# Kernel optimization log

Measured on AMD Instinct MI355X. Metric: run time of the kernel, lower is better.

## Reference

```python
import jax, jax.numpy as jnp
import numpy as np
from jax import lax

DIM = 384
HEADS = 8

def setup_inputs() -> dict:
    key = jax.random.key(0)
    ks = jax.random.split(key, 7)
    B, C, H, W = 4, DIM, 128, 128
    x = jax.random.normal(ks[0], (B, C, H, W), dtype=jnp.float32)
    y = jax.random.normal(ks[1], (B, C, H, W), dtype=jnp.float32)
    s1 = 1.0 / np.sqrt(C)
    Wq = jax.random.normal(ks[2], (C, C), dtype=jnp.float32) * s1          # 1x1 conv [out,in]
    Wkv = jax.random.normal(ks[3], (2 * C, C), dtype=jnp.float32) * s1     # 1x1 conv
    Wdw = jax.random.normal(ks[4], (3 * C, 1, 3, 3), dtype=jnp.float32) * (1.0 / 3.0)  # depthwise 3x3
    Wproj = jax.random.normal(ks[5], (C, C), dtype=jnp.float32) * s1       # 1x1 conv
    temperature = jnp.ones((HEADS, 1, 1), dtype=jnp.float32)
    return {"x": x, "y": y, "Wq": Wq, "Wkv": Wkv, "Wdw": Wdw,
            "Wproj": Wproj, "temperature": temperature}


def _conv1x1(x, W):
    # x: [b,c,h,w], W: [o,c] -> [b,o,h,w]
    return jnp.einsum('bchw,oc->bohw', x, W)


def _l2norm(t, eps=1e-12):
    n = jnp.sqrt(jnp.sum(t * t, axis=-1, keepdims=True))
    return t / jnp.maximum(n, eps)


def reference(x, y, Wq, Wkv, Wdw, Wproj, temperature):
    b, c, h, w = x.shape
    q = _conv1x1(x, Wq)                     # [b,c,h,w]
    kv = _conv1x1(y, Wkv)                   # [b,2c,h,w]
    qkv = jnp.concatenate([q, kv], axis=1)  # [b,3c,h,w]
    qkv = lax.conv_general_dilated(
        qkv, Wdw, window_strides=(1, 1), padding='SAME',
        dimension_numbers=('NCHW', 'OIHW', 'NCHW'),
        feature_group_count=3 * c)
    q, k, v = jnp.split(qkv, 3, axis=1)
    cp = c // HEADS
    hw = h * w
    # b (head c) h w -> b head c (h w)
    q = q.reshape(b, HEADS, cp, hw)
    k = k.reshape(b, HEADS, cp, hw)
    v = v.reshape(b, HEADS, cp, hw)
    q = _l2norm(q)
    k = _l2norm(k)
    attn = jnp.einsum('bhcn,bhdn->bhcd', q, k) * temperature  # [b,head,cp,cp]
    attn = jax.nn.softmax(attn, axis=-1)
    out = jnp.einsum('bhcd,bhdn->bhcn', attn, v)              # [b,head,cp,hw]
    out = out.reshape(b, c, h, w)
    return _conv1x1(out, Wproj)
```

## Files before the change

### kernel.cpp

```cpp
#include <hip/hip_runtime.h>
#include <hip/hip_bf16.h>

#define DIM 384
#define HEADS 8
#define CP 48
#define NB 4
#define HIMG 128
#define WIMG 128
#define HW 16384

using bf16 = __hip_bfloat16;

typedef __attribute__((ext_vector_type(8))) short bf16x8;
typedef __attribute__((ext_vector_type(4))) float f32x4;

__device__ __forceinline__ float lo_bf(unsigned u){ union{unsigned i; float f;} c; c.i = u<<16; return c.f; }
__device__ __forceinline__ float hi_bf(unsigned u){ union{unsigned i; float f;} c; c.i = u & 0xffff0000u; return c.f; }
__device__ __forceinline__ bf16 f2bf(float v){ return __float2bfloat16(v); }
__device__ __forceinline__ unsigned short bfbits(float v){ union{ bf16 h; unsigned short u; } c; c.h = f2bf(v); return c.u; }
__device__ __forceinline__ float s2f(short s){ union{unsigned u; float f;} c; c.u = ((unsigned)(unsigned short)s) << 16; return c.f; }
__device__ __forceinline__ void cvt4(const short* p, float* o){
  uint2 u = *(const uint2*)p;
  o[0]=lo_bf(u.x); o[1]=hi_bf(u.x); o[2]=lo_bf(u.y); o[3]=hi_bf(u.y);
}

__device__ __forceinline__ float4 load4f(const float* p){ return *(const float4*)p; }
__device__ __forceinline__ float4 load4f(const bf16* p){
  uint2 u = *(const uint2*)p;
  float4 r; r.x = lo_bf(u.x); r.y = hi_bf(u.x); r.z = lo_bf(u.y); r.w = hi_bf(u.y); return r;
}

__device__ __forceinline__ void st(float* p, float v){ *p = v; }
__device__ __forceinline__ void st(bf16* p, float v){ *p = f2bf(v); }

#define GLD_LDS16(g, l) __builtin_amdgcn_global_load_lds( \
    (const __attribute__((address_space(1))) void*)(g), \
    (__attribute__((address_space(3))) void*)(l), 16, 0, 0)

__global__ __launch_bounds__(256) void convert_w(
    const float* __restrict__ Wq, const float* __restrict__ Wkv,
    bf16* __restrict__ Wq_bf, bf16* __restrict__ Wkv_bf)
{
  int idx = (blockIdx.x*256 + threadIdx.x) * 2;
  const int NQ = DIM*DIM;
  const int NKV = 2*DIM*DIM;
  if (idx < NQ) {
    unsigned u = (unsigned)bfbits(Wq[idx]) | ((unsigned)bfbits(Wq[idx+1]) << 16);
    *(unsigned*)(Wq_bf + idx) = u;
  } else {
    int j = idx - NQ;
    if (j < NKV) {
      unsigned u = (unsigned)bfbits(Wkv[j]) | ((unsigned)bfbits(Wkv[j+1]) << 16);
      *(unsigned*)(Wkv_bf + j) = u;
    }
  }
}

template<typename TIn>
__global__ __launch_bounds__(256) void transpose_cast(
    const TIn* __restrict__ in0, const TIn* __restrict__ in1,
    bf16* __restrict__ out0, bf16* __restrict__ out1,
    long inBatchStride, long outBatchStride)
{
  const int zb = blockIdx.z;
  const TIn* in = (zb < NB) ? in0 : in1;
  bf16* outp = (zb < NB) ? out0 : out1;
  const int b = zb & 3;
  const int n0 = blockIdx.x * 64;
  const int c0 = blockIdx.y * 64;
  const TIn* inb = in + (long)b * inBatchStride;
  bf16* outb = outp + (long)b * outBatchStride;

  __shared__ float tile[64][66];
  const int t = threadIdx.x;
#pragma unroll
  for (int i = 0; i < 4; ++i) {
    int g = i*256 + t;
    int r = g >> 4, c4 = g & 15;
    float4 v = load4f(inb + (long)(c0 + r)*HW + n0 + c4*4);
    tile[r][c4*4+0] = v.x; tile[r][c4*4+1] = v.y;
    tile[r][c4*4+2] = v.z; tile[r][c4*4+3] = v.w;
  }
  __syncthreads();
#pragma unroll
  for (int i = 0; i < 8; ++i) {
    int g = i*256 + t;
    int n = g >> 5, cu = g & 31;
    unsigned u = (unsigned)bfbits(tile[cu*2][n]) | ((unsigned)bfbits(tile[cu*2+1][n]) << 16);
    *(unsigned*)(outb + (long)(n0 + n)*DIM + c0 + cu*2) = u;
  }
}

template<typename TOut>
__global__ __launch_bounds__(256) void gemm_mfma(
    const bf16* __restrict__ A, long aStride,
    const bf16* __restrict__ Bt, TOut* __restrict__ C, int M, int K)
{
  const int b  = blockIdx.z;
  const int m0 = blockIdx.y * 128;
  const int n0 = blockIdx.x * 128;
  const bf16* Ab  = A  + (long)b * aStride;
  const bf16* Btb = Bt + (long)b * (long)HW * K;
  TOut* Cb = C + (long)b * (long)M * HW;

  __shared__ short As[128*64];
  __shared__ short Bs[128*64];

  const int t = threadIdx.x;
  const int w = t >> 6, lane = t & 63;
  const int quad = lane >> 4, l16 = lane & 15;
  const int wm = (w >> 1) * 64, wn = (w & 1) * 64;

  const bf16* gA[4]; const bf16* gB[4];
#pragma unroll
  for (int i = 0; i < 4; ++i) {
    int f = w*256 + i*64 + lane;
    int r = f >> 3, p = f & 7;
    int c = p ^ (r & 7);
    gA[i] = Ab  + (long)(m0 + r)*K + c*8;
    gB[i] = Btb + (long)(n0 + r)*K + c*8;
  }

  f32x4 acc[4][4] = {};

  for (int k0 = 0; k0 < K; k0 += 64) {
#pragma unroll
    for (int i = 0; i < 4; ++i) {
      GLD_LDS16(gA[i], As + (w*256 + i*64)*8);
      GLD_LDS16(gB[i], Bs + (w*256 + i*64)*8);
      gA[i] += 64; gB[i] += 64;
    }
    __syncthreads();
#pragma unroll
    for (int kk = 0; kk < 2; ++kk) {
      bf16x8 af[4], bfr[4];
      const int sw = (kk*4 + quad) ^ (l16 & 7);
#pragma unroll
      for (int mt = 0; mt < 4; ++mt) {
        af[mt]  = *(const bf16x8*)(As + (wm + mt*16 + l16)*64 + sw*8);
        bfr[mt] = *(const bf16x8*)(Bs + (wn + mt*16 + l16)*64 + sw*8);
      }
#pragma unroll
      for (int mt = 0; mt < 4; ++mt)
#pragma unroll
        for (int nt = 0; nt < 4; ++nt)
          acc[mt][nt] = __builtin_amdgcn_mfma_f32_16x16x32_bf16(af[mt], bfr[nt], acc[mt][nt], 0, 0, 0);
    }
    __syncthreads();
  }

#pragma unroll
  for (int mt = 0; mt < 4; ++mt)
#pragma unroll
    for (int nt = 0; nt < 4; ++nt)
#pragma unroll
      for (int j = 0; j < 4; ++j) {
        int row = m0 + wm + mt*16 + quad*4 + j;
        int col = n0 + wn + nt*16 + l16;
        st(Cb + (long)row*HW + col, acc[mt][nt][j]);
      }
}

__global__ __launch_bounds__(256, 6) void dwconv_inplace(
    bf16* __restrict__ qb, bf16* __restrict__ kvb,
    const float* __restrict__ Wdw, float* __restrict__ ssq)
{
  const int ch = blockIdx.x;
  const int b  = blockIdx.y;
  bf16* plane = (ch < DIM) ? qb + ((long)b*DIM + ch)*HW
                           : kvb + ((long)b*2*DIM + (ch - DIM))*HW;
  float w9[9];
#pragma unroll
  for (int i = 0; i < 9; ++i) w9[i] = Wdw[ch*9 + i];

  __shared__ short t_[66*140];
  __shared__ float wsum[4];
  const int t = threadIdx.x;

  if (t < 66) *(uint2*)&t_[t*140 + 128] = make_uint2(0u, 0u);

#pragma unroll
  for (int i = 0; i < 9; ++i) {
    int chunk = i*256 + t;
    if (chunk < 66*32) {
      int r = chunk >> 5, c8 = chunk & 31;
      int gh = r - 1;
      uint2 v = make_uint2(0u, 0u);
      if (gh >= 0) v = *(const uint2*)(plane + gh*128 + c8*4);
      *(uint2*)&t_[r*140 + c8*4] = v;
    }
  }
  __syncthreads();

  const int r  = t >> 2;
  const int q  = t & 3;
  const int c0 = q * 32;
  float ss = 0.f;
  unsigned outu[16];

  auto compute = [&]() {
    const short* rT = t_ + (r    )*140 + c0;
    const short* rM = t_ + (r + 1)*140 + c0;
    const short* rB = t_ + (r + 2)*140 + c0;
    float at[4], am[4], ab[4];
    cvt4(rT, at); cvt4(rM, am); cvt4(rB, ab);
    float lt, lm, lb;
    if (q == 0) { lt = lm = lb = 0.f; }
    else { lt = s2f(rT[-1]); lm = s2f(rM[-1]); lb = s2f(rB[-1]); }
#pragma unroll
    for (int jb = 0; jb < 32; jb += 4) {
      float bt[4], bm[4], bb[4];
      cvt4(rT + jb + 4, bt);
      cvt4(rM + jb + 4, bm);
      cvt4(rB + jb + 4, bb);
      float o0 = w9[0]*lt    + w9[1]*at[0] + w9[2]*at[1]
               + w9[3]*lm    + w9[4]*am[0] + w9[5]*am[1]
               + w9[6]*lb    + w9[7]*ab[0] + w9[8]*ab[1];
      float o1 = w9[0]*at[0] + w9[1]*at[1] + w9[2]*at[2]
               + w9[3]*am[0] + w9[4]*am[1] + w9[5]*am[2]
               + w9[6]*ab[0] + w9[7]*ab[1] + w9[8]*ab[2];
      float o2 = w9[0]*at[1] + w9[1]*at[2] + w9[2]*at[3]
               + w9[3]*am[1] + w9[4]*am[2] + w9[5]*am[3]
               + w9[6]*ab[1] + w9[7]*ab[2] + w9[8]*ab[3];
      float o3 = w9[0]*at[2] + w9[1]*at[3] + w9[2]*bt[0]
               + w9[3]*am[2] + w9[4]*am[3] + w9[5]*bm[0]
               + w9[6]*ab[2] + w9[7]*ab[3] + w9[8]*bb[0];
      ss += o0*o0 + o1*o1 + o2*o2 + o3*o3;
      outu[(jb>>1)  ] = (unsigned)bfbits(o0) | ((unsigned)bfbits(o1) << 16);
      outu[(jb>>1)+1] = (unsigned)bfbits(o2) | ((unsigned)bfbits(o3) << 16);
      lt = at[3]; lm = am[3]; lb = ab[3];
#pragma unroll
      for (int u2 = 0; u2 < 4; ++u2) { at[u2]=bt[u2]; am[u2]=bm[u2]; ab[u2]=bb[u2]; }
    }
  };

  compute();
  uint2 halo = make_uint2(0u, 0u);
  if (t < 64) halo = *(const uint2*)&t_[(64 + (t >> 5))*140 + (t & 31)*4];
  __syncthreads();

#pragma unroll
  for (int i2 = 0; i2 < 8; ++i2)
    *(uint2*)&t_[r*140 + c0 + i2*4] = *(uint2*)&outu[i2*2];
  __syncthreads();
#pragma unroll
  for (int i2 = 0; i2 < 4; ++i2) {
    int chunk = i2*256 + t;
    int orow = chunk >> 4, ocol = (chunk & 15)*8;
    uint2 lo = *(const uint2*)&t_[orow*140 + ocol];
    uint2 hi = *(const uint2*)&t_[orow*140 + ocol + 4];
    *(uint4*)(plane + (long)orow*128 + ocol) = make_uint4(lo.x, lo.y, hi.x, hi.y);
  }
  __syncthreads();

  if (t < 64) *(uint2*)&t_[(t >> 5)*140 + (t & 31)*4] = halo;
#pragma unroll
  for (int i2 = 0; i2 < 8; ++i2) {
    int chunk = i2*256 + t;
    int rr = chunk >> 5, c8 = chunk & 31;
    int gh = 65 + rr;
    uint2 v = make_uint2(0u, 0u);
    if (gh < 128) v = *(const uint2*)(plane + gh*128 + c8*4);
    *(uint2*)&t_[(rr + 2)*140 + c8*4] = v;
  }
  __syncthreads();

  compute();
  __syncthreads();
#pragma unroll
  for (int i2 = 0; i2 < 8; ++i2)
    *(uint2*)&t_[r*140 + c0 + i2*4] = *(uint2*)&outu[i2*2];
  __syncthreads();
#pragma unroll
  for (int i2 = 0; i2 < 4; ++i2) {
    int chunk = i2*256 + t;
    int orow = chunk >> 4, ocol = (chunk & 15)*8;
    uint2 lo = *(const uint2*)&t_[orow*140 + ocol];
    uint2 hi = *(const uint2*)&t_[orow*140 + ocol + 4];
    *(uint4*)(plane + (long)(64 + orow)*128 + ocol) = make_uint4(lo.x, lo.y, hi.x, hi.y);
  }

  if (ch < 2*DIM) {
#pragma unroll
    for (int off = 32; off; off >>= 1) ss += __shfl_down(ss, off);
    if ((t & 63) == 0) wsum[t >> 6] = ss;
    __syncthreads();
    if (t == 0) ssq[b*2*DIM + ch] = wsum[0]+wsum[1]+wsum[2]+wsum[3];
  }
}

__global__ __launch_bounds__(512) void s_mfma(
    const bf16* __restrict__ qd, const bf16* __restrict__ kd,
    float* __restrict__ Sp)
{
  const int split = blockIdx.x;
  const int h = blockIdx.y, b = blockIdx.z;
  const int t = threadIdx.x, w = t >> 6, lane = t & 63;
  const int quad = lane >> 4, l16 = lane & 15;
  const bf16* qp = qd + ((long)b*DIM + h*CP)*HW;
  const bf16* kp = kd + ((long)b*DIM + h*CP)*HW;
  const int nbase = (split*8 + w) * 256;

  f32x4 acc[3][3] = {};
  for (int ks = 0; ks < 8; ++ks) {
    const int n = nbase + ks*32 + quad*8;
    bf16x8 aq[3], bk[3];
#pragma unroll
    for (int i = 0; i < 3; ++i) {
      aq[i] = *(const bf16x8*)(qp + (long)(i*16 + l16)*HW + n);
      bk[i] = *(const bf16x8*)(kp + (long)(i*16 + l16)*HW + n);
    }
#pragma unroll
    for (int i = 0; i < 3; ++i)
#pragma unroll
      for (int j = 0; j < 3; ++j)
        acc[i][j] = __builtin_amdgcn_mfma_f32_16x16x32_bf16(aq[i], bk[j], acc[i][j], 0, 0, 0);
  }

  __shared__ float Sred[8][CP*CP];
#pragma unroll
  for (int i = 0; i < 3; ++i)
#pragma unroll
    for (int j = 0; j < 3; ++j)
#pragma unroll
      for (int rr = 0; rr < 4; ++rr)
        Sred[w][(i*16 + quad*4 + rr)*CP + j*16 + l16] = acc[i][j][rr];
  __syncthreads();

  float* out = Sp + (long)split*(NB*HEADS*CP*CP) + ((long)(b*HEADS + h))*CP*CP;
  for (int g = t; g < CP*CP; g += 512) {
    float s = 0.f;
#pragma unroll
    for (int ww = 0; ww < 8; ++ww) s += Sred[ww][g];
    out[g] = s;
  }
}

__global__ __launch_bounds__(64) void softmax_attn(
    float* __restrict__ Sp, const float* __restrict__ ssq,
    const float* __restrict__ temp)
{
  const int bhc = blockIdx.x;
  const int c = bhc % CP;
  const int h = (bhc / CP) % HEADS;
  const int b = bhc / (CP * HEADS);
  const int lane = threadIdx.x;
  const long rowoff = ((long)(b*HEADS + h))*CP*CP + c*CP;
  const float rq = rsqrtf(ssq[b*2*DIM + h*CP + c]);
  const float tmp = temp[h];
  float logit = -1e30f;
  if (lane < CP) {
    float s = 0.f;
#pragma unroll
    for (int sl = 0; sl < 8; ++sl) s += Sp[(long)sl*(NB*HEADS*CP*CP) + rowoff + lane];
    float rk = rsqrtf(ssq[b*2*DIM + DIM + h*CP + lane]);
    logit = s * rq * rk * tmp;
  }
  float m = logit;
#pragma unroll
  for (int off = 32; off; off >>= 1) m = fmaxf(m, __shfl_down(m, off));
  m = __shfl(m, 0);
  float e = (lane < CP) ? __expf(logit - m) : 0.f;
  float s = e;
#pragma unroll
  for (int off = 32; off; off >>= 1) s += __shfl_down(s, off);
  s = __shfl(s, 0);
  if (lane < CP) Sp[rowoff + lane] = e / s;
}

__global__ __launch_bounds__(256) void w2fold(
    const float* __restrict__ attn, const float* __restrict__ Wproj,
    bf16* __restrict__ W2)
{
  const int ot = blockIdx.x;
  const int h  = blockIdx.y;
  const int b  = blockIdx.z;
  __shared__ float at[CP][CP];
  __shared__ float wp[128][CP];
  const int t = threadIdx.x;
  const float* Ap = attn + ((long)(b*HEADS + h))*CP*CP;
#pragma unroll
  for (int i = 0; i < 9; ++i) {
    int idx = t + 256*i;
    at[idx / CP][idx % CP] = Ap[idx];
  }
#pragma unroll
  for (int i = 0; i < 24; ++i) {
    int idx = t + 256*i;
    int o = idx / CP, c = idx % CP;
    wp[o][c] = Wproj[(long)(ot*128 + o)*DIM + h*CP + c];
  }
  __syncthreads();
#pragma unroll
  for (int i = 0; i < 24; ++i) {
    int idx = t + 256*i;
    int o = idx / CP, d = idx % CP;
    float a = 0.f;
#pragma unroll
    for (int c = 0; c < CP; ++c) a += wp[o][c] * at[c][d];
    W2[((long)b*DIM + ot*128 + o)*DIM + h*CP + d] = f2bf(a);
  }
}

extern "C" void kernel_launch(void* const* d_in, const int* in_sizes, int n_in,
                              void* d_out, int out_size, void* d_ws, size_t ws_size,
                              hipStream_t stream) {
  const float* x     = (const float*)d_in[0];
  const float* y     = (const float*)d_in[1];
  const float* Wq    = (const float*)d_in[2];
  const float* Wkv   = (const float*)d_in[3];
  const float* Wdw   = (const float*)d_in[4];
  const float* Wproj = (const float*)d_in[5];
  const float* temp  = (const float*)d_in[6];
  float* out = (float*)d_out;

  char* ws = (char*)d_ws;
  const long SZ_T  = 50331648L;
  bf16* xT    = (bf16*)(ws + 0L);
  bf16* yT    = (bf16*)(ws + SZ_T);
  bf16* q_bf  = (bf16*)(ws + 2*SZ_T);
  bf16* kv_bf = (bf16*)(ws + 3*SZ_T);
  char* tail  = ws + 5*SZ_T;
  bf16* Wq_bf  = (bf16*)(tail);
  bf16* Wkv_bf = (bf16*)(tail + 294912L);
  float* Sp    = (float*)(tail);
  bf16* W2_bf  = (bf16*)(tail + 294912L);
  float* ssq   = (float*)(tail + 2359296L);
  bf16* vdT    = xT;
  bf16* vd     = kv_bf + (long)DIM*HW;

  convert_w<<<864, 256, 0, stream>>>(Wq, Wkv, Wq_bf, Wkv_bf);
  transpose_cast<float><<<dim3(HW/64, DIM/64, 8), 256, 0, stream>>>(
      x, y, xT, yT, (long)DIM*HW, (long)HW*DIM);
  gemm_mfma<bf16><<<dim3(HW/128, DIM/128, NB), 256, 0, stream>>>(
      Wq_bf, 0, xT, q_bf, DIM, DIM);
  gemm_mfma<bf16><<<dim3(HW/128, 2*DIM/128, NB), 256, 0, stream>>>(
      Wkv_bf, 0, yT, kv_bf, 2*DIM, DIM);
  dwconv_inplace<<<dim3(3*DIM, NB), 256, 0, stream>>>(q_bf, kv_bf, Wdw, ssq);
  transpose_cast<bf16><<<dim3(HW/64, DIM/64, NB), 256, 0, stream>>>(
      vd, nullptr, vdT, nullptr, (long)2*DIM*HW, (long)HW*DIM);
  s_mfma<<<dim3(8, HEADS, NB), 512, 0, stream>>>(q_bf, kv_bf, Sp);
  softmax_attn<<<dim3(NB*HEADS*CP), 64, 0, stream>>>(Sp, ssq, temp);
  w2fold<<<dim3(3, HEADS, NB), 256, 0, stream>>>(Sp, Wproj, W2_bf);
  gemm_mfma<float><<<dim3(HW/128, DIM/128, NB), 256, 0, stream>>>(
      W2_bf, (long)DIM*DIM, vdT, out, DIM, DIM);
}
```

Baseline: 568.3 us.

## Process whole dwconv plane in one pass with 512 threads and direct stores

The depthwise conv kernel now loads the full 128x128 bf16 plane plus zero halo into shared memory at once, using 512 threads, instead of two 64-row halves with halo carry-over. Each thread computes its 32 outputs and writes them straight to global memory as 16-byte stores, with no staging back through shared memory. This removes several barriers and the second load/compute phase. In exchange, shared memory per block grows to about 36 KB, which can limit how many blocks fit per CU. Padding the row with a left zero column removes the q==0 branch.

```diff
diff --git a/kernel.cpp b/kernel.cpp
--- a/kernel.cpp
+++ b/kernel.cpp
@@ -161,7 +161,7 @@
       }
 }
 
-__global__ __launch_bounds__(256, 6) void dwconv_inplace(
+__global__ __launch_bounds__(512, 8) void dwconv_inplace(
     bf16* __restrict__ qb, bf16* __restrict__ kvb,
     const float* __restrict__ Wdw, float* __restrict__ ssq)
 {
@@ -173,111 +173,78 @@
 #pragma unroll
   for (int i = 0; i < 9; ++i) w9[i] = Wdw[ch*9 + i];
 
-  __shared__ short t_[66*140];
-  __shared__ float wsum[4];
+  __shared__ short t_[130*140];
+  __shared__ float wsum[8];
   const int t = threadIdx.x;
 
-  if (t < 66) *(uint2*)&t_[t*140 + 128] = make_uint2(0u, 0u);
-
-#pragma unroll
-  for (int i = 0; i < 9; ++i) {
-    int chunk = i*256 + t;
-    if (chunk < 66*32) {
-      int r = chunk >> 5, c8 = chunk & 31;
-      int gh = r - 1;
-      uint2 v = make_uint2(0u, 0u);
-      if (gh >= 0) v = *(const uint2*)(plane + gh*128 + c8*4);
-      *(uint2*)&t_[r*140 + c8*4] = v;
-    }
+  uint2 v[8];
+#pragma unroll
+  for (int i = 0; i < 8; ++i) {
+    int chunk = i*512 + t;
+    int r = chunk >> 5, c8 = chunk & 31;
+    v[i] = *(const uint2*)(plane + r*128 + c8*4);
+  }
+
+  if (t < 74) {
+    int row = (t < 37) ? 0 : 129;
+    int c4 = (t < 37) ? t : (t - 37);
+    *(uint2*)&t_[row*140 + c4*4] = make_uint2(0u, 0u);
+  }
+  if (t < 128)
+    *(uint2*)&t_[(t+1)*140] = make_uint2(0u, 0u);
+  {
+    if (t < 256) {
+      int row = (t >> 1) + 1, half = t & 1;
+      *(uint2*)&t_[row*140 + 132 + half*4] = make_uint2(0u, 0u);
+    }
+  }
+
+#pragma unroll
+  for (int i = 0; i < 8; ++i) {
+    int chunk = i*512 + t;
+    int r = chunk >> 5, c8 = chunk & 31;
+    *(uint2*)&t_[(r+1)*140 + 4 + c8*4] = v[i];
   }
   __syncthreads();
 
-  const int r  = t >> 2;
-  const int q  = t & 3;
+  const int r = t >> 2, q = t & 3;
   const int c0 = q * 32;
+  const short* rT = t_ + (r    )*140 + 4 + c0;
+  const short* rM = t_ + (r + 1)*140 + 4 + c0;
+  const short* rB = t_ + (r + 2)*140 + 4 + c0;
+
+  float at[4], am[4], ab[4];
+  cvt4(rT, at); cvt4(rM, am); cvt4(rB, ab);
+  float lt = s2f(rT[-1]), lm = s2f(rM[-1]), lb = s2f(rB[-1]);
+
   float ss = 0.f;
-  unsigned outu[16];
-
-  auto compute = [&]() {
-    const short* rT = t_ + (r    )*140 + c0;
-    const short* rM = t_ + (r + 1)*140 + c0;
-    const short* rB = t_ + (r + 2)*140 + c0;
-    float at[4], am[4], ab[4];
-    cvt4(rT, at); cvt4(rM, am); cvt4(rB, ab);
-    float lt, lm, lb;
-    if (q == 0) { lt = lm = lb = 0.f; }
-    else { lt = s2f(rT[-1]); lm = s2f(rM[-1]); lb = s2f(rB[-1]); }
-#pragma unroll
-    for (int jb = 0; jb < 32; jb += 4) {
-      float bt[4], bm[4], bb[4];
-      cvt4(rT + jb + 4, bt);
-      cvt4(rM + jb + 4, bm);
-      cvt4(rB + jb + 4, bb);
-      float o0 = w9[0]*lt    + w9[1]*at[0] + w9[2]*at[1]
-               + w9[3]*lm    + w9[4]*am[0] + w9[5]*am[1]
-               + w9[6]*lb    + w9[7]*ab[0] + w9[8]*ab[1];
-      float o1 = w9[0]*at[0] + w9[1]*at[1] + w9[2]*at[2]
-               + w9[3]*am[0] + w9[4]*am[1] + w9[5]*am[2]
-               + w9[6]*ab[0] + w9[7]*ab[1] + w9[8]*ab[2];
-      float o2 = w9[0]*at[1] + w9[1]*at[2] + w9[2]*at[3]
-               + w9[3]*am[1] + w9[4]*am[2] + w9[5]*am[3]
-               + w9[6]*ab[1] + w9[7]*ab[2] + w9[8]*ab[3];
-      float o3 = w9[0]*at[2] + w9[1]*at[3] + w9[2]*bt[0]
-               + w9[3]*am[2] + w9[4]*am[3] + w9[5]*bm[0]
-               + w9[6]*ab[2] + w9[7]*ab[3] + w9[8]*bb[0];
-      ss += o0*o0 + o1*o1 + o2*o2 + o3*o3;
-      outu[(jb>>1)  ] = (unsigned)bfbits(o0) | ((unsigned)bfbits(o1) << 16);
-      outu[(jb>>1)+1] = (unsigned)bfbits(o2) | ((unsigned)bfbits(o3) << 16);
-      lt = at[3]; lm = am[3]; lb = ab[3];
-#pragma unroll
-      for (int u2 = 0; u2 < 4; ++u2) { at[u2]=bt[u2]; am[u2]=bm[u2]; ab[u2]=bb[u2]; }
-    }
-  };
-
-  compute();
-  uint2 halo = make_uint2(0u, 0u);
-  if (t < 64) halo = *(const uint2*)&t_[(64 + (t >> 5))*140 + (t & 31)*4];
-  __syncthreads();
-
-#pragma unroll
-  for (int i2 = 0; i2 < 8; ++i2)
-    *(uint2*)&t_[r*140 + c0 + i2*4] = *(uint2*)&outu[i2*2];
-  __syncthreads();
-#pragma unroll
-  for (int i2 = 0; i2 < 4; ++i2) {
-    int chunk = i2*256 + t;
-    int orow = chunk >> 4, ocol = (chunk & 15)*8;
-    uint2 lo = *(const uint2*)&t_[orow*140 + ocol];
-    uint2 hi = *(const uint2*)&t_[orow*140 + ocol + 4];
-    *(uint4*)(plane + (long)orow*128 + ocol) = make_uint4(lo.x, lo.y, hi.x, hi.y);
-  }
-  __syncthreads();
-
-  if (t < 64) *(uint2*)&t_[(t >> 5)*140 + (t & 31)*4] = halo;
-#pragma unroll
-  for (int i2 = 0; i2 < 8; ++i2) {
-    int chunk = i2*256 + t;
-    int rr = chunk >> 5, c8 = chunk & 31;
-    int gh = 65 + rr;
-    uint2 v = make_uint2(0u, 0u);
-    if (gh < 128) v = *(const uint2*)(plane + gh*128 + c8*4);
-    *(uint2*)&t_[(rr + 2)*140 + c8*4] = v;
-  }
-  __syncthreads();
-
-  compute();
-  __syncthreads();
-#pragma unroll
-  for (int i2 = 0; i2 < 8; ++i2)
-    *(uint2*)&t_[r*140 + c0 + i2*4] = *(uint2*)&outu[i2*2];
-  __syncthreads();
-#pragma unroll
-  for (int i2 = 0; i2 < 4; ++i2) {
-    int chunk = i2*256 + t;
-    int orow = chunk >> 4, ocol = (chunk & 15)*8;
-    uint2 lo = *(const uint2*)&t_[orow*140 + ocol];
-    uint2 hi = *(const uint2*)&t_[orow*140 + ocol + 4];
-    *(uint4*)(plane + (long)(64 + orow)*128 + ocol) = make_uint4(lo.x, lo.y, hi.x, hi.y);
+  unsigned p0 = 0, p1 = 0;
+#pragma unroll
+  for (int jb = 0; jb < 32; jb += 4) {
+    float bt[4], bm[4], bb[4];
+    cvt4(rT + jb + 4, bt);
+    cvt4(rM + jb + 4, bm);
+    cvt4(rB + jb + 4, bb);
+    float o0 = w9[0]*lt    + w9[1]*at[0] + w9[2]*at[1]
+             + w9[3]*lm    + w9[4]*am[0] + w9[5]*am[1]
+             + w9[6]*lb    + w9[7]*ab[0] + w9[8]*ab[1];
+    float o1 = w9[0]*at[0] + w9[1]*at[1] + w9[2]*at[2]
+             + w9[3]*am[0] + w9[4]*am[1] + w9[5]*am[2]
+             + w9[6]*ab[0] + w9[7]*ab[1] + w9[8]*ab[2];
+    float o2 = w9[0]*at[1] + w9[1]*at[2] + w9[2]*at[3]
+             + w9[3]*am[1] + w9[4]*am[2] + w9[5]*am[3]
+             + w9[6]*ab[1] + w9[7]*ab[2] + w9[8]*ab[3];
+    float o3 = w9[0]*at[2] + w9[1]*at[3] + w9[2]*bt[0]
+             + w9[3]*am[2] + w9[4]*am[3] + w9[5]*bm[0]
+             + w9[6]*ab[2] + w9[7]*ab[3] + w9[8]*bb[0];
+    ss += o0*o0 + o1*o1 + o2*o2 + o3*o3;
+    unsigned u0 = (unsigned)bfbits(o0) | ((unsigned)bfbits(o1) << 16);
+    unsigned u1 = (unsigned)bfbits(o2) | ((unsigned)bfbits(o3) << 16);
+    if ((jb & 4) == 0) { p0 = u0; p1 = u1; }
+    else *(uint4*)(plane + r*128 + c0 + (jb - 4)) = make_uint4(p0, p1, u0, u1);
+    lt = at[3]; lm = am[3]; lb = ab[3];
+#pragma unroll
+    for (int u2 = 0; u2 < 4; ++u2) { at[u2]=bt[u2]; am[u2]=bm[u2]; ab[u2]=bb[u2]; }
   }
 
   if (ch < 2*DIM) {
@@ -285,7 +252,12 @@
     for (int off = 32; off; off >>= 1) ss += __shfl_down(ss, off);
     if ((t & 63) == 0) wsum[t >> 6] = ss;
     __syncthreads();
-    if (t == 0) ssq[b*2*DIM + ch] = wsum[0]+wsum[1]+wsum[2]+wsum[3];
+    if (t == 0) {
+      float s = 0.f;
+#pragma unroll
+      for (int i = 0; i < 8; ++i) s += wsum[i];
+      ssq[b*2*DIM + ch] = s;
+    }
   }
 }
 
@@ -436,7 +408,7 @@
       Wq_bf, 0, xT, q_bf, DIM, DIM);
   gemm_mfma<bf16><<<dim3(HW/128, 2*DIM/128, NB), 256, 0, stream>>>(
       Wkv_bf, 0, yT, kv_bf, 2*DIM, DIM);
-  dwconv_inplace<<<dim3(3*DIM, NB), 256, 0, stream>>>(q_bf, kv_bf, Wdw, ssq);
+  dwconv_inplace<<<dim3(3*DIM, NB), 512, 0, stream>>>(q_bf, kv_bf, Wdw, ssq);
   transpose_cast<bf16><<<dim3(HW/64, DIM/64, NB), 256, 0, stream>>>(
       vd, nullptr, vdT, nullptr, (long)2*DIM*HW, (long)HW*DIM);
   s_mfma<<<dim3(8, HEADS, NB), 512, 0, stream>>>(q_bf, kv_bf, Sp);
```

After: 495.7 us. 12.8% less time.
